# Performance work log

Hardware: AMD Instinct MI355X
Metric: run time of the kernel (lower is better)

## Reference

```python
import jax, jax.numpy as jnp
import numpy as np

B, S, D, NH, DH, L, FF, IMG, WH, DC = 4, 8320, 512, 8, 64, 4, 2048, 128, 65, 8


def _ln(x, g, b, eps=1e-5):
    m = jnp.mean(x, axis=-1, keepdims=True)
    v = jnp.mean((x - m) ** 2, axis=-1, keepdims=True)
    return (x - m) * jax.lax.rsqrt(v + eps) * g + b


def _pos_encoding(coords, d_half):
    # 2D sinusoidal PE: half channels encode col, half encode row (FIT PositionalEncoding2D)
    d_ax = d_half // 2
    div = jnp.exp(-jnp.arange(0, d_ax, 2, dtype=jnp.float32) * (np.log(10000.0) / d_ax))

    def enc(p):
        a = p[:, None].astype(jnp.float32) * div[None, :]
        return jnp.stack([jnp.sin(a), jnp.cos(a)], -1).reshape(p.shape[0], d_ax)

    return jnp.concatenate([enc(coords[:, 1]), enc(coords[:, 0])], -1)  # (S, d_half)


def setup_inputs():
    key = jax.random.key(0)
    ks = iter(jax.random.split(key, 64))
    n = lambda shape, s=0.02: jax.random.normal(next(ks), shape, jnp.float32) * s
    rows, cols = jnp.meshgrid(jnp.arange(IMG), jnp.arange(WH), indexing='ij')
    coords = jnp.stack([rows.reshape(-1), cols.reshape(-1)], -1).astype(jnp.int32)  # (S,2)
    return dict(
        x=jax.random.normal(next(ks), (B, S, 2), jnp.float32),
        fbp=jax.random.normal(next(ks), (B, S, 2), jnp.float32),
        mag_min=jnp.zeros((1,), jnp.float32),
        mag_max=jnp.ones((1,), jnp.float32),
        attenuation=jax.random.uniform(next(ks), (1, IMG, WH), jnp.float32),
        coords=coords,
        dst_flatten_coords=jnp.arange(S, dtype=jnp.int32),
        img_shape=IMG,
        emb_w=n((2, D // 2), 0.5), emb_b=jnp.zeros((D // 2,), jnp.float32),
        Wq=n((L, D, D)), bq=jnp.zeros((L, D), jnp.float32),
        Wk=n((L, D, D)), bk=jnp.zeros((L, D), jnp.float32),
        Wv=n((L, D, D)), bv=jnp.zeros((L, D), jnp.float32),
        Wo=n((L, D, D)), bo=jnp.zeros((L, D), jnp.float32),
        ln1_g=jnp.ones((L, D), jnp.float32), ln1_b=jnp.zeros((L, D), jnp.float32),
        W1=n((L, D, FF)), b1=jnp.zeros((L, FF), jnp.float32),
        W2=n((L, FF, D)), b2=jnp.zeros((L, D), jnp.float32),
        ln2_g=jnp.ones((L, D), jnp.float32), ln2_b=jnp.zeros((L, D), jnp.float32),
        lnf_g=jnp.ones((D,), jnp.float32), lnf_b=jnp.zeros((D,), jnp.float32),
        amp_w=n((D, 1)), amp_b=jnp.zeros((1,), jnp.float32),
        phase_w=n((D, 1)), phase_b=jnp.zeros((1,), jnp.float32),
        conv1_w=n((DC, 1, 3, 3), 0.1), conv1_b=jnp.zeros((DC,), jnp.float32),
        bn_g=jnp.ones((DC,), jnp.float32), bn_b=jnp.zeros((DC,), jnp.float32),
        conv2_w=n((1, DC, 1, 1), 0.1), conv2_b=jnp.zeros((1,), jnp.float32),
    )


def _conv(x, w, b, pad):
    y = jax.lax.conv_general_dilated(x, w, (1, 1), [(pad, pad), (pad, pad)],
                                     dimension_numbers=('NCHW', 'OIHW', 'NCHW'))
    return y + b[None, :, None, None]


def _forward(fbp, mag_min, mag_max, attenuation,
             emb_w, emb_b, Wq, bq, Wk, bk, Wv, bv, Wo, bo,
             ln1_g, ln1_b, W1, b1, W2, b2, ln2_g, ln2_b, lnf_g, lnf_b,
             amp_w, amp_b, phase_w, phase_b,
             conv1_w, conv1_b, bn_g, bn_b, conv2_w, conv2_b,
             coords, dst_flatten_coords, img_shape):
    pe = _pos_encoding(coords, D // 2)  # (S, D/2)
    h = jnp.concatenate([fbp @ emb_w + emb_b,
                         jnp.broadcast_to(pe, (fbp.shape[0], S, D // 2))], -1)  # (B,S,D)
    for i in range(L):
        # non-causal linear attention (fast-transformers): phi(x)=elu(x)+1
        q = (h @ Wq[i] + bq[i]).reshape(B, S, NH, DH)
        k = (h @ Wk[i] + bk[i]).reshape(B, S, NH, DH)
        v = (h @ Wv[i] + bv[i]).reshape(B, S, NH, DH)
        qf = jax.nn.elu(q) + 1.0
        kf = jax.nn.elu(k) + 1.0
        kv = jnp.einsum('bshd,bshm->bhdm', kf, v)
        z = 1.0 / (jnp.einsum('bshd,bhd->bsh', qf, kf.sum(1)) + 1e-6)
        att = jnp.einsum('bshd,bhdm,bsh->bshm', qf, kv, z).reshape(B, S, D)
        h = _ln(h + (att @ Wo[i] + bo[i]), ln1_g[i], ln1_b[i])      # post-norm
        y = jax.nn.relu(h @ W1[i] + b1[i]) @ W2[i] + b2[i]
        h = _ln(h + y, ln2_g[i], ln2_b[i])
    h = _ln(h, lnf_g, lnf_b)  # final encoder LayerNorm
    y_amp = h @ amp_w + amp_b
    y_phase = jnp.tanh(h @ phase_w + phase_b)
    y_hat = jnp.concatenate([y_amp, y_phase], -1)  # (B,S,2)
    # convert2DFT: denormalize amp/phase, scatter into flattened half-spectrum
    amp = jnp.exp((y_hat[..., 0] + 1.0) * 0.5 * (mag_max - mag_min) + mag_min)
    phi = y_hat[..., 1] * jnp.pi
    dft_flat = amp * jnp.cos(phi) + 1j * (amp * jnp.sin(phi))
    dft = jnp.zeros((B, IMG * WH), jnp.complex64).at[:, dst_flatten_coords].set(dft_flat.astype(jnp.complex64))
    dft = dft.reshape(B, IMG, WH) * attenuation
    img = jnp.fft.irfftn(dft, s=(IMG, IMG), axes=(1, 2))
    img = jnp.roll(img, (IMG // 2, IMG // 2), (1, 2))[:, None]  # (B,1,IMG,IMG)
    # conv + (training-mode) batchnorm refinement with residual
    c = jax.nn.relu(_conv(img, conv1_w, conv1_b, 1))
    m = jnp.mean(c, axis=(0, 2, 3), keepdims=True)
    var = jnp.mean((c - m) ** 2, axis=(0, 2, 3), keepdims=True)
    c = (c - m) * jax.lax.rsqrt(var + 1e-5) * bn_g[None, :, None, None] + bn_b[None, :, None, None]
    c = _conv(c, conv2_w, conv2_b, 0)
    img_post = c + img
    return y_hat, img_post[:, 0]


def reference(x, fbp, mag_min, mag_max, attenuation, coords, dst_flatten_coords, img_shape,
              emb_w, emb_b, Wq, bq, Wk, bk, Wv, bv, Wo, bo,
              ln1_g, ln1_b, W1, b1, W2, b2, ln2_g, ln2_b, lnf_g, lnf_b,
              amp_w, amp_b, phase_w, phase_b,
              conv1_w, conv1_b, bn_g, bn_b, conv2_w, conv2_b):
    # x is accepted (matches original forward signature) but unused by the module body
    return _forward(fbp, mag_min, mag_max, attenuation,
                    emb_w, emb_b, Wq, bq, Wk, bk, Wv, bv, Wo, bo,
                    ln1_g, ln1_b, W1, b1, W2, b2, ln2_g, ln2_b, lnf_g, lnf_b,
                    amp_w, amp_b, phase_w, phase_b,
                    conv1_w, conv1_b, bn_g, bn_b, conv2_w, conv2_b,
                    coords, dst_flatten_coords, img_shape)
```

## Files before the change

### kernel.cpp

```cpp
#include <hip/hip_runtime.h>
#include <math.h>

#define NB 4
#define SS 8320
#define DD 512
#define NH_ 8
#define LL 4
#define FF_ 2048
#define MTOT (NB*SS)

typedef __attribute__((ext_vector_type(8))) short short8;
typedef __attribute__((ext_vector_type(4))) float f32x4;

__device__ __forceinline__ unsigned short f2bf(float f){
  union { float f; unsigned int u; } x; x.f = f;
  unsigned int r = x.u + 0x7FFFu + ((x.u >> 16) & 1u);
  return (unsigned short)(r >> 16);
}
__device__ __forceinline__ float bf2f(unsigned short u){
  return __uint_as_float(((unsigned int)u) << 16);
}
__device__ __forceinline__ void gload_lds16(const void* g, void* l){
  __builtin_amdgcn_global_load_lds(
      (__attribute__((address_space(1))) void*)g,
      (__attribute__((address_space(3))) void*)l, 16, 0, 0);
}
__device__ __forceinline__ float wred(float v){
  #pragma unroll
  for (int o = 32; o; o >>= 1) v += __shfl_xor(v, o);
  return v;
}
__device__ __forceinline__ float block_sum256(float v){
  __shared__ float sb[4];
  #pragma unroll
  for (int o = 32; o; o >>= 1) v += __shfl_down(v, o);
  int w = threadIdx.x >> 6;
  __syncthreads();
  if ((threadIdx.x & 63) == 0) sb[w] = v;
  __syncthreads();
  return sb[0] + sb[1] + sb[2] + sb[3];
}

struct P4 { const float* p0; const float* p1; const float* p2; const float* p3; };

__global__ __launch_bounds__(256) void transpose4_kernel(P4 srcs, unsigned short* __restrict__ dst)
{
  __shared__ float tile[32][33];
  const int z = blockIdx.z;
  const float* src = (z == 0) ? srcs.p0 : (z == 1) ? srcs.p1 : (z == 2) ? srcs.p2 : srcs.p3;
  unsigned short* d = dst + (size_t)z * DD * DD;
  const int n0 = blockIdx.x * 32, k0 = blockIdx.y * 32;
  const int tx = threadIdx.x & 31, ty = threadIdx.x >> 5;
  #pragma unroll
  for (int j = 0; j < 32; j += 8) tile[ty + j][tx] = src[(size_t)(k0 + ty + j) * DD + n0 + tx];
  __syncthreads();
  #pragma unroll
  for (int j = 0; j < 32; j += 8) d[(size_t)(n0 + ty + j) * DD + k0 + tx] = f2bf(tile[tx][ty + j]);
}

__global__ __launch_bounds__(256) void transpose_bf16_kernel(
    const float* __restrict__ src, unsigned short* __restrict__ dst, int K, int N)
{
  __shared__ float tile[32][33];
  const int n0 = blockIdx.x * 32, k0 = blockIdx.y * 32;
  const int tx = threadIdx.x & 31, ty = threadIdx.x >> 5;
  #pragma unroll
  for (int j = 0; j < 32; j += 8) tile[ty + j][tx] = src[(size_t)(k0 + ty + j) * N + n0 + tx];
  __syncthreads();
  #pragma unroll
  for (int j = 0; j < 32; j += 8) dst[(size_t)(n0 + ty + j) * K + k0 + tx] = f2bf(tile[tx][ty + j]);
}

__global__ __launch_bounds__(256) void embed_kernel(
    const float* __restrict__ fbp, const int* __restrict__ coords,
    const float* __restrict__ emb_w, const float* __restrict__ emb_b,
    unsigned short* __restrict__ hb)
{
  const int row = blockIdx.x;
  const int c = threadIdx.x;
  const int s = row % SS;
  const float f0 = fbp[(size_t)row * 2], f1 = fbp[(size_t)row * 2 + 1];
  const float v0 = f0 * emb_w[c] + f1 * emb_w[256 + c] + emb_b[c];
  const int p = (c < 128) ? coords[s * 2 + 1] : coords[s * 2];
  const int c2 = c & 127;
  const int jj = c2 >> 1;
  const float dv = expf(-(float)(2 * jj) * (9.210340371976184f / 128.f));
  const float a = (float)p * dv;
  const float v1 = (c2 & 1) ? cosf(a) : sinf(a);
  const size_t base = (size_t)row * DD;
  hb[base + c] = f2bf(v0);
  hb[base + 256 + c] = f2bf(v1);
}

__global__ __launch_bounds__(256) void gemm_qkv_kernel(
    const unsigned short* __restrict__ A,
    const unsigned short* __restrict__ Bt,
    const float* __restrict__ bq_, const float* __restrict__ bk_, const float* __restrict__ bv_,
    unsigned short* __restrict__ qo, unsigned short* __restrict__ ko, unsigned short* __restrict__ vo)
{
  __shared__ __attribute__((aligned(16))) unsigned short As[128 * 64];
  __shared__ __attribute__((aligned(16))) unsigned short Bs[128 * 64];
  const int tid = threadIdx.x;
  const int lane = tid & 63, w = tid >> 6;
  const int lr = lane & 15, lg = lane >> 4;
  const int wm = w >> 1, wn = w & 1;
  const int bn = blockIdx.x, bm = blockIdx.y;
  const int which = bn >> 2;
  const unsigned short* Ag = A + (size_t)bm * 128 * DD;
  const unsigned short* Bg = Bt + (size_t)bn * 128 * DD;
  unsigned short* out = (which == 0) ? qo : (which == 1) ? ko : vo;
  const float* bias = (which == 0) ? bq_ : (which == 1) ? bk_ : bv_;
  f32x4 acc[4][4] = {};
  for (int kt = 0; kt < 8; ++kt) {
    if (kt) __syncthreads();
    const int kbase = kt << 6;
    #pragma unroll
    for (int i = 0; i < 4; ++i) {
      int cid = i * 256 + tid;
      int row = cid >> 3, c = cid & 7;
      gload_lds16(Ag + (size_t)row * DD + kbase + ((c ^ (row & 7)) << 3), (void*)(As + cid * 8));
    }
    #pragma unroll
    for (int i = 0; i < 4; ++i) {
      int cid = i * 256 + tid;
      int row = cid >> 3, c = cid & 7;
      gload_lds16(Bg + (size_t)row * DD + kbase + ((c ^ (row & 7)) << 3), (void*)(Bs + cid * 8));
    }
    __syncthreads();
    #pragma unroll
    for (int kk = 0; kk < 2; ++kk) {
      short8 af[4], bfv[4];
      #pragma unroll
      for (int f = 0; f < 4; ++f) {
        int row = wm * 64 + f * 16 + lr;
        af[f] = *(const short8*)(As + row * 64 + (((kk * 4 + lg) ^ (row & 7)) << 3));
      }
      #pragma unroll
      for (int f = 0; f < 4; ++f) {
        int row = wn * 64 + f * 16 + lr;
        bfv[f] = *(const short8*)(Bs + row * 64 + (((kk * 4 + lg) ^ (row & 7)) << 3));
      }
      #pragma unroll
      for (int fm = 0; fm < 4; ++fm)
        #pragma unroll
        for (int fn = 0; fn < 4; ++fn)
          acc[fm][fn] = __builtin_amdgcn_mfma_f32_16x16x32_bf16(af[fm], bfv[fn], acc[fm][fn], 0, 0, 0);
    }
  }
  const int elu = (which < 2);
  #pragma unroll
  for (int fm = 0; fm < 4; ++fm) {
    const int row0 = bm * 128 + wm * 64 + fm * 16 + lg * 4;
    #pragma unroll
    for (int fn = 0; fn < 4; ++fn) {
      const int col = (bn & 3) * 128 + wn * 64 + fn * 16 + lr;
      const float bv = bias[col];
      #pragma unroll
      for (int r = 0; r < 4; ++r) {
        float v = acc[fm][fn][r] + bv;
        if (elu) v = (v > 0.f) ? (v + 1.f) : expf(v);
        out[(size_t)(row0 + r) * DD + col] = f2bf(v);
      }
    }
  }
}

template<int ACT, int RES>
__global__ __launch_bounds__(256) void gemm_kernel(
    const unsigned short* __restrict__ A,
    const unsigned short* __restrict__ Bt,
    const float* __restrict__ bias,
    unsigned short* __restrict__ C,
    int N, int K, int lda, int ldb)
{
  __shared__ __attribute__((aligned(16))) unsigned short As[128 * 64];
  __shared__ __attribute__((aligned(16))) unsigned short Bs[128 * 64];
  const int tid = threadIdx.x;
  const int lane = tid & 63, w = tid >> 6;
  const int lr = lane & 15, lg = lane >> 4;
  const int wm = w >> 1, wn = w & 1;
  const int bn = blockIdx.x, bm = blockIdx.y;
  const unsigned short* Ag = A + (size_t)bm * 128 * lda;
  const unsigned short* Bg = Bt + (size_t)bn * 128 * ldb;
  f32x4 acc[4][4] = {};
  const int nkt = K >> 6;
  for (int kt = 0; kt < nkt; ++kt) {
    if (kt) __syncthreads();
    const int kbase = kt << 6;
    #pragma unroll
    for (int i = 0; i < 4; ++i) {
      int cid = i * 256 + tid;
      int row = cid >> 3, c = cid & 7;
      gload_lds16(Ag + (size_t)row * lda + kbase + ((c ^ (row & 7)) << 3), (void*)(As + cid * 8));
    }
    #pragma unroll
    for (int i = 0; i < 4; ++i) {
      int cid = i * 256 + tid;
      int row = cid >> 3, c = cid & 7;
      gload_lds16(Bg + (size_t)row * ldb + kbase + ((c ^ (row & 7)) << 3), (void*)(Bs + cid * 8));
    }
    __syncthreads();
    #pragma unroll
    for (int kk = 0; kk < 2; ++kk) {
      short8 af[4], bfv[4];
      #pragma unroll
      for (int f = 0; f < 4; ++f) {
        int row = wm * 64 + f * 16 + lr;
        af[f] = *(const short8*)(As + row * 64 + (((kk * 4 + lg) ^ (row & 7)) << 3));
      }
      #pragma unroll
      for (int f = 0; f < 4; ++f) {
        int row = wn * 64 + f * 16 + lr;
        bfv[f] = *(const short8*)(Bs + row * 64 + (((kk * 4 + lg) ^ (row & 7)) << 3));
      }
      #pragma unroll
      for (int fm = 0; fm < 4; ++fm)
        #pragma unroll
        for (int fn = 0; fn < 4; ++fn)
          acc[fm][fn] = __builtin_amdgcn_mfma_f32_16x16x32_bf16(af[fm], bfv[fn], acc[fm][fn], 0, 0, 0);
    }
  }
  #pragma unroll
  for (int fm = 0; fm < 4; ++fm) {
    const int row0 = bm * 128 + wm * 64 + fm * 16 + lg * 4;
    #pragma unroll
    for (int fn = 0; fn < 4; ++fn) {
      const int col = bn * 128 + wn * 64 + fn * 16 + lr;
      const float bv = bias[col];
      #pragma unroll
      for (int r = 0; r < 4; ++r) {
        float v = acc[fm][fn][r] + bv;
        if (ACT == 2) v = (v > 0.f) ? v : 0.f;
        const size_t idx = (size_t)(row0 + r) * N + col;
        if (RES) v += bf2f(C[idx]);
        C[idx] = f2bf(v);
      }
    }
  }
}

__global__ __launch_bounds__(256) void kv_part_kernel(
    const unsigned short* __restrict__ kb, const unsigned short* __restrict__ vb,
    float* __restrict__ kvp, float* __restrict__ ksp)
{
  __shared__ __attribute__((aligned(16))) float Kc[128][64];
  __shared__ __attribute__((aligned(16))) float Vc[128][64];
  const int ch = blockIdx.x;
  const int bh = blockIdx.y;
  const int NBH = gridDim.y;
  const int b = bh >> 3, h = bh & 7;
  const int tid = threadIdx.x;
  const int d = tid >> 2, m0 = (tid & 3) << 4;
  f32x4 a0 = {}, a1 = {}, a2 = {}, a3 = {};
  float sk = 0.f;
  for (int t = 0; t < 5; ++t) {
    if (t) __syncthreads();
    const size_t roff = ((size_t)b * SS + ch * 640 + t * 128) * DD + h * 64;
    #pragma unroll
    for (int i = 0; i < 8; ++i) {
      int e4 = i * 256 + tid;
      int r = e4 >> 4, c4 = e4 & 15;
      ushort4 kq = *(const ushort4*)(kb + roff + (size_t)r * DD + c4 * 4);
      ushort4 vq = *(const ushort4*)(vb + roff + (size_t)r * DD + c4 * 4);
      f32x4 kf4 = { bf2f(kq.x), bf2f(kq.y), bf2f(kq.z), bf2f(kq.w) };
      f32x4 vf4 = { bf2f(vq.x), bf2f(vq.y), bf2f(vq.z), bf2f(vq.w) };
      *(f32x4*)&Kc[r][c4 * 4] = kf4;
      *(f32x4*)&Vc[r][c4 * 4] = vf4;
    }
    __syncthreads();
    for (int s2 = 0; s2 < 128; ++s2) {
      const float kd = Kc[s2][d];
      const f32x4* vp = (const f32x4*)&Vc[s2][m0];
      a0 += kd * vp[0]; a1 += kd * vp[1]; a2 += kd * vp[2]; a3 += kd * vp[3];
    }
    if (tid < 64) {
      for (int s2 = 0; s2 < 128; ++s2) sk += Kc[s2][tid];
    }
  }
  float* ko = kvp + (((size_t)ch * NBH + bh) * 64 + d) * 64 + m0;
  *(f32x4*)(ko) = a0; *(f32x4*)(ko + 4) = a1; *(f32x4*)(ko + 8) = a2; *(f32x4*)(ko + 12) = a3;
  if (tid < 64) ksp[((size_t)ch * NBH + bh) * 64 + tid] = sk;
}

__global__ __launch_bounds__(256) void kv_reduce_kernel(
    const float* __restrict__ kvp, const float* __restrict__ ksp,
    unsigned short* __restrict__ kvT, float* __restrict__ ksum, int NBH)
{
  const int idx = blockIdx.x * 256 + threadIdx.x;
  const int nkv = NBH * 4096;
  if (idx < nkv) {
    const int bh = idx >> 12, dm = idx & 4095;
    const int d = dm >> 6, m = dm & 63;
    float s = 0.f;
    #pragma unroll
    for (int c = 0; c < 13; ++c) s += kvp[(((size_t)c * NBH + bh) << 12) + dm];
    kvT[(size_t)bh * 4096 + m * 64 + d] = f2bf(s);
  } else if (idx < nkv + NBH * 64) {
    const int i2 = idx - nkv;
    const int bh = i2 >> 6, d = i2 & 63;
    float s = 0.f;
    #pragma unroll
    for (int c = 0; c < 13; ++c) s += ksp[((size_t)c * NBH + bh) * 64 + d];
    ksum[i2] = s;
  }
}

__global__ __launch_bounds__(256) void z_kernel(
    const unsigned short* __restrict__ qb, const float* __restrict__ ksum,
    float* __restrict__ z, int M)
{
  const int idx = blockIdx.x * 256 + threadIdx.x;
  if (idx >= M * NH_) return;
  const int h = idx & 7;
  const int bs = idx >> 3;
  const int b = bs / SS;
  const unsigned short* q = qb + (size_t)bs * DD + h * 64;
  const float* ks = ksum + ((size_t)(b * 8 + h)) * 64;
  float acc = 0.f;
  #pragma unroll
  for (int j = 0; j < 16; ++j) {
    ushort4 qv = *(const ushort4*)(q + j * 4);
    acc += bf2f(qv.x) * ks[j * 4] + bf2f(qv.y) * ks[j * 4 + 1]
         + bf2f(qv.z) * ks[j * 4 + 2] + bf2f(qv.w) * ks[j * 4 + 3];
  }
  z[idx] = 1.f / (acc + 1e-6f);
}

__global__ __launch_bounds__(256) void attn_kernel(
    unsigned short* __restrict__ qb, const unsigned short* __restrict__ kvT,
    const float* __restrict__ z)
{
  __shared__ __attribute__((aligned(16))) unsigned short Qs[128 * 64];
  __shared__ __attribute__((aligned(16))) unsigned short Ks[64 * 64];
  const int st = blockIdx.x;
// ... 141 lines not shown
  const int tid = threadIdx.x;
  if (tid < 128) {
    float a = (float)tid * (3.14159265358979323846f / 64.f);
    ct[tid] = cosf(a); st[tid] = sinf(a);
  }
  __syncthreads();
  const int idx = blockIdx.x * 256 + tid;
  const int v = idx % 65;
  const int y = (idx / 65) & 127;
  const int b = idx / (65 * 128);
  const float* pr = dre + (size_t)b * SS + v;
  const float* pi = dimg + (size_t)b * SS + v;
  float ar = 0.f, ai = 0.f;
  for (int u = 0; u < 128; ++u) {
    int t2 = (u * y) & 127;
    float cr = ct[t2], si = st[t2];
    float xr = pr[(size_t)u * 65], xi = pi[(size_t)u * 65];
    ar += xr * cr - xi * si;
    ai += xr * si + xi * cr;
  }
  tre[idx] = ar * (1.f / 128.f);
  tim[idx] = ai * (1.f / 128.f);
}

__global__ __launch_bounds__(256) void fftB_kernel(
    const float* __restrict__ tre, const float* __restrict__ tim,
    float* __restrict__ img)
{
  __shared__ float ct[128], st[128];
  const int tid = threadIdx.x;
  if (tid < 128) {
    float a = (float)tid * (3.14159265358979323846f / 64.f);
    ct[tid] = cosf(a); st[tid] = sinf(a);
  }
  __syncthreads();
  const int idx = blockIdx.x * 256 + tid;
  const int x = idx & 127;
  const int y = (idx >> 7) & 127;
  const int b = idx >> 14;
  const float* pr = tre + ((size_t)b * 128 + y) * 65;
  const float* pi = tim + ((size_t)b * 128 + y) * 65;
  float a2 = pr[0] + ((x & 1) ? -pr[64] : pr[64]);
  for (int v = 1; v < 64; ++v) {
    int t2 = (v * x) & 127;
    a2 += 2.f * (pr[v] * ct[t2] - pi[v] * st[t2]);
  }
  a2 *= (1.f / 128.f);
  const int yy = (y + 64) & 127, xx = (x + 64) & 127;
  img[((size_t)b << 14) + (yy << 7) + xx] = a2;
}

__global__ __launch_bounds__(256) void conv1_kernel(
    const float* __restrict__ img, const float* __restrict__ w,
    const float* __restrict__ bi, float* __restrict__ c1)
{
  const int idx = blockIdx.x * 256 + threadIdx.x;
  const int x = idx & 127, y = (idx >> 7) & 127, ch = (idx >> 14) & 7, b = idx >> 17;
  const float* ip = img + ((size_t)b << 14);
  const float* wp = w + ch * 9;
  float acc = bi[ch];
  #pragma unroll
  for (int dy = -1; dy <= 1; ++dy) {
    const int yy = y + dy;
    if (yy < 0 || yy > 127) continue;
    #pragma unroll
    for (int dx = -1; dx <= 1; ++dx) {
      const int xx = x + dx;
      if (xx < 0 || xx > 127) continue;
      acc += ip[(yy << 7) + xx] * wp[(dy + 1) * 3 + (dx + 1)];
    }
  }
  c1[idx] = acc > 0.f ? acc : 0.f;
}

__global__ __launch_bounds__(256) void bn_part_kernel(
    const float* __restrict__ c1, float* __restrict__ bnp)
{
  const int ch = blockIdx.x >> 5, sl = blockIdx.x & 31;
  const int tid = threadIdx.x;
  const int n = sl * 2048 + tid * 8;
  const int b = n >> 14, i = n & 16383;
  const float* p = c1 + (((size_t)b * 8 + ch) << 14) + i;
  float4 a0 = *(const float4*)p, a1 = *(const float4*)(p + 4);
  float s = a0.x + a0.y + a0.z + a0.w + a1.x + a1.y + a1.z + a1.w;
  float sq = a0.x*a0.x + a0.y*a0.y + a0.z*a0.z + a0.w*a0.w
           + a1.x*a1.x + a1.y*a1.y + a1.z*a1.z + a1.w*a1.w;
  s = block_sum256(s);
  sq = block_sum256(sq);
  if (tid == 0) { bnp[blockIdx.x] = s; bnp[256 + blockIdx.x] = sq; }
}

__global__ __launch_bounds__(256) void bn_final_kernel(
    const float* __restrict__ bnp, float* __restrict__ stats)
{
  const int t = threadIdx.x;
  float s = bnp[t], sq = bnp[256 + t];
  #pragma unroll
  for (int o = 16; o; o >>= 1) { s += __shfl_down(s, o, 32); sq += __shfl_down(sq, o, 32); }
  if ((t & 31) == 0) {
    const int ch = t >> 5;
    const float m = s * (1.f / 65536.f);
    const float var = sq * (1.f / 65536.f) - m * m;
    stats[ch] = m;
    stats[8 + ch] = rsqrtf(var + 1e-5f);
  }
}

__global__ __launch_bounds__(256) void conv2_kernel(
    const float* __restrict__ c1, const float* __restrict__ stats,
    const float* __restrict__ bng, const float* __restrict__ bnb,
    const float* __restrict__ w2, const float* __restrict__ b2,
    const float* __restrict__ img, float* __restrict__ out)
{
  const int idx = blockIdx.x * 256 + threadIdx.x;
  const int b = idx >> 14, sp = idx & 16383;
  float acc = b2[0];
  #pragma unroll
  for (int ch = 0; ch < 8; ++ch) {
    float v = c1[(((size_t)b * 8 + ch) << 14) + sp];
    v = (v - stats[ch]) * stats[8 + ch] * bng[ch] + bnb[ch];
    acc += v * w2[ch];
  }
  out[idx] = acc + img[idx];
}

extern "C" void kernel_launch(void* const* d_in, const int* in_sizes, int n_in,
                              void* d_out, int out_size, void* d_ws, size_t ws_size,
                              hipStream_t stream)
{
  (void)in_sizes; (void)n_in; (void)out_size;
  const float* fbp = (const float*)d_in[1];
  const float* mag_min = (const float*)d_in[2];
  const float* mag_max = (const float*)d_in[3];
  const float* atten = (const float*)d_in[4];
  const int* coords = (const int*)d_in[5];
  const int* dstc = (const int*)d_in[6];
  const float* emb_w = (const float*)d_in[8];
  const float* emb_b = (const float*)d_in[9];
  const float* Wq = (const float*)d_in[10]; const float* bq = (const float*)d_in[11];
  const float* Wk = (const float*)d_in[12]; const float* bk = (const float*)d_in[13];
  const float* Wv = (const float*)d_in[14]; const float* bv = (const float*)d_in[15];
  const float* Wo = (const float*)d_in[16]; const float* bo = (const float*)d_in[17];
  const float* ln1g = (const float*)d_in[18]; const float* ln1b = (const float*)d_in[19];
  const float* W1 = (const float*)d_in[20]; const float* b1 = (const float*)d_in[21];
  const float* W2 = (const float*)d_in[22]; const float* b2 = (const float*)d_in[23];
  const float* ln2g = (const float*)d_in[24]; const float* ln2b = (const float*)d_in[25];
  const float* lnfg = (const float*)d_in[26]; const float* lnfb = (const float*)d_in[27];
  const float* aw = (const float*)d_in[28]; const float* ab = (const float*)d_in[29];
  const float* pw = (const float*)d_in[30]; const float* pb = (const float*)d_in[31];
  const float* c1w = (const float*)d_in[32]; const float* c1b = (const float*)d_in[33];
  const float* bng = (const float*)d_in[34]; const float* bnb = (const float*)d_in[35];
  const float* c2w = (const float*)d_in[36]; const float* c2b = (const float*)d_in[37];

  auto rnd = [](size_t b_) { return (b_ + 255) & ~(size_t)255; };
  const size_t SZ_M   = rnd((size_t)MTOT * DD * 2);
  const size_t SZ_Y1  = rnd((size_t)MTOT * FF_ * 2);
  const size_t SZ_WT  = rnd((size_t)4 * DD * DD * 2);
  const size_t SZ_W12 = rnd((size_t)DD * FF_ * 2);
  const size_t NEED_FULL = 4 * SZ_M + rnd((size_t)13*32*4096*4) + rnd((size_t)13*32*64*4) +
                           rnd((size_t)32*4096*2) + rnd((size_t)32*64*4) +
                           rnd((size_t)MTOT*NH_*4) + SZ_WT + 2*SZ_W12 + 4096;
  const size_t NEED_FULLY = NEED_FULL + SZ_Y1;
  const size_t NEED_FB = SZ_M + rnd((size_t)SS*DD*2) + rnd((size_t)SS*FF_*2) +
                         rnd((size_t)8*4096*2) + rnd((size_t)8*64*4) +
                         rnd((size_t)SS*NH_*4) + SZ_WT + 2*SZ_W12 + 4096;
  const int mode = (ws_size >= NEED_FULLY) ? 2 : (ws_size >= NEED_FULL) ? 1 : 0;
  if (mode == 0 && ws_size < NEED_FB) return;

  char* wsp = (char*)d_ws;
  size_t off = 0;
  auto alloc = [&](size_t bytes) -> char* { char* p = wsp + off; off += rnd(bytes); return p; };

  unsigned short *hb, *qb_, *kb_, *vb_, *y1c, *y1ded = nullptr, *kvT, *wsT, *w1T, *w2T;
  float *kvp, *ksp, *ksum, *zb;
  if (mode >= 1) {
    hb  = (unsigned short*)alloc((size_t)MTOT * DD * 2);
    qb_ = (unsigned short*)alloc((size_t)MTOT * DD * 2);
    kb_ = (unsigned short*)alloc((size_t)MTOT * DD * 2);
    vb_ = (unsigned short*)alloc((size_t)MTOT * DD * 2);
    if (mode == 2) y1ded = (unsigned short*)alloc((size_t)MTOT * FF_ * 2);
    kvp = (float*)alloc((size_t)13 * 32 * 4096 * 4);
    ksp = (float*)alloc((size_t)13 * 32 * 64 * 4);
    kvT = (unsigned short*)alloc((size_t)32 * 4096 * 2);
    ksum = (float*)alloc((size_t)32 * 64 * 4);
    zb  = (float*)alloc((size_t)MTOT * NH_ * 4);
    y1c = nullptr;
  } else {
    hb  = (unsigned short*)alloc((size_t)MTOT * DD * 2);
    qb_ = (unsigned short*)alloc((size_t)SS * DD * 2);
    unsigned short* uni = (unsigned short*)alloc((size_t)SS * FF_ * 2);
    kb_ = uni;
    vb_ = uni + (size_t)SS * DD;
    kvp = (float*)(uni + 2 * (size_t)SS * DD);
    ksp = kvp + (size_t)13 * 8 * 4096;
    kvT = (unsigned short*)alloc((size_t)8 * 4096 * 2);
    ksum = (float*)alloc((size_t)8 * 64 * 4);
    zb  = (float*)alloc((size_t)SS * NH_ * 4);
    y1c = uni;
  }
  wsT = (unsigned short*)alloc((size_t)4 * DD * DD * 2);
  w1T = (unsigned short*)alloc((size_t)DD * FF_ * 2);
  w2T = (unsigned short*)alloc((size_t)DD * FF_ * 2);

  float* dre  = (float*)qb_;
  float* dimg = dre + (size_t)NB * SS;
  float* tre  = dimg + (size_t)NB * SS;
  float* tim  = tre + (size_t)NB * 128 * 65;
  float* img  = tim + (size_t)NB * 128 * 65;
  float* c1buf = img + (size_t)NB * 128 * 128;
  float* bnp  = c1buf + (size_t)NB * 8 * 128 * 128;
  float* stats = bnp + 512;

  embed_kernel<<<MTOT, 256, 0, stream>>>(fbp, coords, emb_w, emb_b, hb);

  const int npass = (mode >= 1) ? 1 : 4;
  const int NBH = (mode >= 1) ? 32 : 8;
  const int Mrows = (mode >= 1) ? MTOT : SS;

  for (int i = 0; i < LL; ++i) {
    P4 sq4 = { Wq + (size_t)i * DD * DD, Wk + (size_t)i * DD * DD,
               Wv + (size_t)i * DD * DD, Wo + (size_t)i * DD * DD };
    transpose4_kernel<<<dim3(16, 16, 4), 256, 0, stream>>>(sq4, wsT);
    transpose_bf16_kernel<<<dim3(64, 16), 256, 0, stream>>>(W1 + (size_t)i * DD * FF_, w1T, DD, FF_);
    transpose_bf16_kernel<<<dim3(16, 64), 256, 0, stream>>>(W2 + (size_t)i * DD * FF_, w2T, FF_, DD);

    for (int p = 0; p < npass; ++p) {
      unsigned short* hbp = hb + (size_t)p * SS * DD;
      gemm_qkv_kernel<<<dim3(12, Mrows / 128), 256, 0, stream>>>(
          hbp, wsT, bq + (size_t)i * DD, bk + (size_t)i * DD, bv + (size_t)i * DD,
          qb_, kb_, vb_);
      kv_part_kernel<<<dim3(13, NBH), 256, 0, stream>>>(kb_, vb_, kvp, ksp);
      kv_reduce_kernel<<<(NBH * 4096 + NBH * 64 + 255) / 256, 256, 0, stream>>>(kvp, ksp, kvT, ksum, NBH);
      z_kernel<<<(Mrows * NH_ + 255) / 256, 256, 0, stream>>>(qb_, ksum, zb, Mrows);
      attn_kernel<<<dim3(65, NBH), 256, 0, stream>>>(qb_, kvT, zb);
      gemm_kernel<0, 1><<<dim3(4, Mrows / 128), 256, 0, stream>>>(
          qb_, wsT + (size_t)3 * DD * DD, bo + (size_t)i * DD, hbp, DD, DD, DD, DD);
      ln_wave_kernel<<<Mrows / 4, 256, 0, stream>>>(hbp, ln1g + (size_t)i * DD, ln1b + (size_t)i * DD);

      if (mode == 2) {
        gemm_kernel<2, 0><<<dim3(16, MTOT / 128), 256, 0, stream>>>(
            hb, w1T, b1 + (size_t)i * FF_, y1ded, FF_, DD, DD, DD);
        gemm_kernel<0, 1><<<dim3(4, MTOT / 128), 256, 0, stream>>>(
            y1ded, w2T, b2 + (size_t)i * DD, hb, DD, FF_, FF_, FF_);
      } else if (mode == 1) {
        unsigned short* y1half = qb_;
        for (int g2 = 0; g2 < 2; ++g2) {
          unsigned short* hbg = hb + (size_t)g2 * 2 * SS * DD;
          gemm_kernel<2, 0><<<dim3(16, 2 * SS / 128), 256, 0, stream>>>(
              hbg, w1T, b1 + (size_t)i * FF_, y1half, FF_, DD, DD, DD);
          gemm_kernel<0, 1><<<dim3(4, 2 * SS / 128), 256, 0, stream>>>(
              y1half, w2T, b2 + (size_t)i * DD, hbg, DD, FF_, FF_, FF_);
        }
      } else {
        gemm_kernel<2, 0><<<dim3(16, SS / 128), 256, 0, stream>>>(
            hbp, w1T, b1 + (size_t)i * FF_, y1c, FF_, DD, DD, DD);
        gemm_kernel<0, 1><<<dim3(4, SS / 128), 256, 0, stream>>>(
            y1c, w2T, b2 + (size_t)i * DD, hbp, DD, FF_, FF_, FF_);
      }
      ln_wave_kernel<<<Mrows / 4, 256, 0, stream>>>(hbp, ln2g + (size_t)i * DD, ln2b + (size_t)i * DD);
    }
  }

  (void)hipMemsetAsync(dre, 0, (size_t)NB * SS * 4 * 2, stream);
  head_wave_kernel<<<MTOT / 4, 256, 0, stream>>>(hb, lnfg, lnfb, aw, ab, pw, pb,
                                                 mag_min, mag_max, atten, dstc,
                                                 (float*)d_out, dre, dimg);
  fftA_kernel<<<130, 256, 0, stream>>>(dre, dimg, tre, tim);
  fftB_kernel<<<256, 256, 0, stream>>>(tre, tim, img);
  conv1_kernel<<<2048, 256, 0, stream>>>(img, c1w, c1b, c1buf);
  bn_part_kernel<<<256, 256, 0, stream>>>(c1buf, bnp);
  bn_final_kernel<<<1, 256, 0, stream>>>(bnp, stats);
  conv2_kernel<<<256, 256, 0, stream>>>(c1buf, stats, bng, bnb, c2w, c2b, img,
                                        (float*)d_out + (size_t)MTOT * 2);
}
```

Before: 2.129 ms.

## Use 256x256 tiled 512-thread GEMMs with XCD remap and hoist weight transposes

Adds new GEMM kernels with 256x256 output tiles, 512 threads, 128KB of dynamic LDS double-buffered with swizzled direct-to-LDS loads, and block-ID remapping so neighbouring tiles land on the same XCD. They replace the 128-tile QKV, output-projection and FFN GEMMs in the full-batch modes. The aim is more reuse of each loaded tile and better L2 locality. All per-layer weight transposes are hoisted into three launches before the layer loop, which adds workspace for all layers' transposed weights. Large tiles risk lower occupancy and wave-quantization tails, since MTOT/256 gives 130 row blocks.

```diff
diff --git a/kernel.cpp b/kernel.cpp
--- a/kernel.cpp
+++ b/kernel.cpp
@@ -43,11 +43,13 @@
 
 struct P4 { const float* p0; const float* p1; const float* p2; const float* p3; };
 
-__global__ __launch_bounds__(256) void transpose4_kernel(P4 srcs, unsigned short* __restrict__ dst)
+__global__ __launch_bounds__(256) void transpose_qkvo_kernel(P4 srcs, unsigned short* __restrict__ dst)
 {
   __shared__ float tile[32][33];
   const int z = blockIdx.z;
-  const float* src = (z == 0) ? srcs.p0 : (z == 1) ? srcs.p1 : (z == 2) ? srcs.p2 : srcs.p3;
+  const int layer = z >> 2, m = z & 3;
+  const float* base = (m == 0) ? srcs.p0 : (m == 1) ? srcs.p1 : (m == 2) ? srcs.p2 : srcs.p3;
+  const float* src = base + (size_t)layer * DD * DD;
   unsigned short* d = dst + (size_t)z * DD * DD;
   const int n0 = blockIdx.x * 32, k0 = blockIdx.y * 32;
   const int tx = threadIdx.x & 31, ty = threadIdx.x >> 5;
@@ -59,9 +61,11 @@
 }
 
 __global__ __launch_bounds__(256) void transpose_bf16_kernel(
-    const float* __restrict__ src, unsigned short* __restrict__ dst, int K, int N)
+    const float* __restrict__ src0, unsigned short* __restrict__ dst0, int K, int N)
 {
   __shared__ float tile[32][33];
+  const float* src = src0 + (size_t)blockIdx.z * K * N;
+  unsigned short* dst = dst0 + (size_t)blockIdx.z * K * N;
   const int n0 = blockIdx.x * 32, k0 = blockIdx.y * 32;
   const int tx = threadIdx.x & 31, ty = threadIdx.x >> 5;
   #pragma unroll
@@ -90,6 +94,188 @@
   const size_t base = (size_t)row * DD;
   hb[base + c] = f2bf(v0);
   hb[base + 256 + c] = f2bf(v1);
+}
+
+__device__ __forceinline__ void xcd_remap(int gx, int gy, int& bn, int& bm)
+{
+  const int nblk = gx * gy;
+  const int id = blockIdx.x + gx * blockIdx.y;
+  const int qd = nblk >> 3, rd = nblk & 7;
+  const int xcd = id & 7, pos = id >> 3;
+  const int nid = (xcd < rd) ? (xcd * (qd + 1) + pos)
+                             : (rd * (qd + 1) + (xcd - rd) * qd + pos);
+  bn = nid % gx; bm = nid / gx;
+}
+
+__device__ __forceinline__ void stage256(const unsigned short* __restrict__ G,
+                                         int ld, int kbase, unsigned short* L, int tid)
+{
+  #pragma unroll
+  for (int i = 0; i < 4; ++i) {
+    int s = i * 512 + tid;
+    int row = s >> 3, cs = s & 7;
+    int c = cs ^ (row & 7);
+    gload_lds16(G + (size_t)row * ld + kbase + (c << 3), (void*)(L + s * 8));
+  }
+}
+
+template<int ACT, int RES>
+__global__ __launch_bounds__(512) void gemm256_kernel(
+    const unsigned short* __restrict__ A,
+    const unsigned short* __restrict__ Bt,
+    const float* __restrict__ bias,
+    unsigned short* __restrict__ C,
+    int N, int K, int lda, int ldb)
+{
+  extern __shared__ __attribute__((aligned(16))) unsigned short smem[];
+  const int tid = threadIdx.x;
+  const int lane = tid & 63, w = tid >> 6;
+  const int lr = lane & 15, lg = lane >> 4;
+  const int wm = w >> 2, wn = w & 3;
+  int bn, bm; xcd_remap(gridDim.x, gridDim.y, bn, bm);
+  const unsigned short* Ag = A + (size_t)bm * 256 * lda;
+  const unsigned short* Bg = Bt + (size_t)bn * 256 * ldb;
+  f32x4 acc[8][4] = {};
+  const int nkt = K >> 6;
+  stage256(Ag, lda, 0, smem, tid);
+  stage256(Bg, ldb, 0, smem + 32768, tid);
+  __syncthreads();
+  for (int kt = 0; kt < nkt; ++kt) {
+    const int so = (kt & 1) << 14;
+    if (kt + 1 < nkt) {
+      const int sn = ((kt + 1) & 1) << 14;
+      stage256(Ag, lda, (kt + 1) << 6, smem + sn, tid);
+      stage256(Bg, ldb, (kt + 1) << 6, smem + 32768 + sn, tid);
+    }
+    const unsigned short* Ab = smem + so;
+    const unsigned short* Bb = smem + 32768 + so;
+    #pragma unroll
+    for (int q = 0; q < 4; ++q) {
+      const int qm = q >> 1, qn = q & 1;
+      short8 af[4][2], bf_[2][2];
+      #pragma unroll
+      for (int f = 0; f < 4; ++f) {
+        int row = wm * 128 + (qm * 4 + f) * 16 + lr;
+        #pragma unroll
+        for (int ks = 0; ks < 2; ++ks)
+          af[f][ks] = *(const short8*)(Ab + row * 64 + (((ks * 4 + lg) ^ (row & 7)) << 3));
+      }
+      #pragma unroll
+      for (int f = 0; f < 2; ++f) {
+        int row = wn * 64 + (qn * 2 + f) * 16 + lr;
+        #pragma unroll
+        for (int ks = 0; ks < 2; ++ks)
+          bf_[f][ks] = *(const short8*)(Bb + row * 64 + (((ks * 4 + lg) ^ (row & 7)) << 3));
+      }
+      __builtin_amdgcn_s_setprio(1);
+      #pragma unroll
+      for (int f = 0; f < 4; ++f)
+        #pragma unroll
+        for (int g2 = 0; g2 < 2; ++g2)
+          #pragma unroll
+          for (int ks = 0; ks < 2; ++ks)
+            acc[qm * 4 + f][qn * 2 + g2] = __builtin_amdgcn_mfma_f32_16x16x32_bf16(
+                af[f][ks], bf_[g2][ks], acc[qm * 4 + f][qn * 2 + g2], 0, 0, 0);
+      __builtin_amdgcn_s_setprio(0);
+    }
+    __syncthreads();
+  }
+  #pragma unroll
+  for (int fm = 0; fm < 8; ++fm) {
+    const int row0 = bm * 256 + wm * 128 + fm * 16 + lg * 4;
+    #pragma unroll
+    for (int fn = 0; fn < 4; ++fn) {
+      const int col = bn * 256 + wn * 64 + fn * 16 + lr;
+      const float bv = bias[col];
+      #pragma unroll
+      for (int r = 0; r < 4; ++r) {
+        float v = acc[fm][fn][r] + bv;
+        if (ACT == 2) v = (v > 0.f) ? v : 0.f;
+        const size_t idx = (size_t)(row0 + r) * N + col;
+        if (RES) v += bf2f(C[idx]);
+        C[idx] = f2bf(v);
+      }
+    }
+  }
+}
+
+__global__ __launch_bounds__(512) void qkv256_kernel(
+    const unsigned short* __restrict__ A,
+    const unsigned short* __restrict__ Bt,
+    const float* __restrict__ bq_, const float* __restrict__ bk_, const float* __restrict__ bv_,
+    unsigned short* __restrict__ qo, unsigned short* __restrict__ ko, unsigned short* __restrict__ vo)
+{
+  extern __shared__ __attribute__((aligned(16))) unsigned short smem[];
+  const int tid = threadIdx.x;
+  const int lane = tid & 63, w = tid >> 6;
+  const int lr = lane & 15, lg = lane >> 4;
+  const int wm = w >> 2, wn = w & 3;
+  int bn, bm; xcd_remap(gridDim.x, gridDim.y, bn, bm);
+  const int which = bn >> 1;
+  unsigned short* out = (which == 0) ? qo : (which == 1) ? ko : vo;
+  const float* bias = (which == 0) ? bq_ : (which == 1) ? bk_ : bv_;
+  const int elu = (which < 2);
+  const unsigned short* Ag = A + (size_t)bm * 256 * DD;
+  const unsigned short* Bg = Bt + (size_t)bn * 256 * DD;
+  f32x4 acc[8][4] = {};
+  stage256(Ag, DD, 0, smem, tid);
+  stage256(Bg, DD, 0, smem + 32768, tid);
+  __syncthreads();
+  for (int kt = 0; kt < 8; ++kt) {
+    const int so = (kt & 1) << 14;
+    if (kt + 1 < 8) {
+      const int sn = ((kt + 1) & 1) << 14;
+      stage256(Ag, DD, (kt + 1) << 6, smem + sn, tid);
+      stage256(Bg, DD, (kt + 1) << 6, smem + 32768 + sn, tid);
+    }
+    const unsigned short* Ab = smem + so;
+    const unsigned short* Bb = smem + 32768 + so;
+    #pragma unroll
+    for (int q = 0; q < 4; ++q) {
+      const int qm = q >> 1, qn = q & 1;
+      short8 af[4][2], bf_[2][2];
+      #pragma unroll
+      for (int f = 0; f < 4; ++f) {
+        int row = wm * 128 + (qm * 4 + f) * 16 + lr;
+        #pragma unroll
+        for (int ks = 0; ks < 2; ++ks)
+          af[f][ks] = *(const short8*)(Ab + row * 64 + (((ks * 4 + lg) ^ (row & 7)) << 3));
+      }
+      #pragma unroll
+      for (int f = 0; f < 2; ++f) {
+        int row = wn * 64 + (qn * 2 + f) * 16 + lr;
+        #pragma unroll
+        for (int ks = 0; ks < 2; ++ks)
+          bf_[f][ks] = *(const short8*)(Bb + row * 64 + (((ks * 4 + lg) ^ (row & 7)) << 3));
+      }
+      __builtin_amdgcn_s_setprio(1);
+      #pragma unroll
+      for (int f = 0; f < 4; ++f)
+        #pragma unroll
+        for (int g2 = 0; g2 < 2; ++g2)
+          #pragma unroll
+          for (int ks = 0; ks < 2; ++ks)
+            acc[qm * 4 + f][qn * 2 + g2] = __builtin_amdgcn_mfma_f32_16x16x32_bf16(
+                af[f][ks], bf_[g2][ks], acc[qm * 4 + f][qn * 2 + g2], 0, 0, 0);
+      __builtin_amdgcn_s_setprio(0);
+    }
+    __syncthreads();
+  }
+  #pragma unroll
+  for (int fm = 0; fm < 8; ++fm) {
+    const int row0 = bm * 256 + wm * 128 + fm * 16 + lg * 4;
+    #pragma unroll
+    for (int fn = 0; fn < 4; ++fn) {
+      const int colr = (bn & 1) * 256 + wn * 64 + fn * 16 + lr;
+      const float bv = bias[colr];
+      #pragma unroll
+      for (int r = 0; r < 4; ++r) {
+        float v = acc[fm][fn][r] + bv;
+        if (elu) v = (v > 0.f) ? (v + 1.f) : expf(v);
+        out[(size_t)(row0 + r) * DD + colr] = f2bf(v);
+      }
+    }
+  }
 }
 
 __global__ __launch_bounds__(256) void gemm_qkv_kernel(
@@ -627,18 +813,26 @@
   const float* bng = (const float*)d_in[34]; const float* bnb = (const float*)d_in[35];
   const float* c2w = (const float*)d_in[36]; const float* c2b = (const float*)d_in[37];
 
+  (void)hipFuncSetAttribute((const void*)&qkv256_kernel,
+        hipFuncAttributeMaxDynamicSharedMemorySize, 131072);
+  (void)hipFuncSetAttribute((const void*)&gemm256_kernel<0, 1>,
+        hipFuncAttributeMaxDynamicSharedMemorySize, 131072);
+  (void)hipFuncSetAttribute((const void*)&gemm256_kernel<2, 0>,
+        hipFuncAttributeMaxDynamicSharedMemorySize, 131072);
+
   auto rnd = [](size_t b_) { return (b_ + 255) & ~(size_t)255; };
-  const size_t SZ_M   = rnd((size_t)MTOT * DD * 2);
-  const size_t SZ_Y1  = rnd((size_t)MTOT * FF_ * 2);
-  const size_t SZ_WT  = rnd((size_t)4 * DD * DD * 2);
-  const size_t SZ_W12 = rnd((size_t)DD * FF_ * 2);
-  const size_t NEED_FULL = 4 * SZ_M + rnd((size_t)13*32*4096*4) + rnd((size_t)13*32*64*4) +
+  const size_t SZ_M    = rnd((size_t)MTOT * DD * 2);
+  const size_t SZ_Y1   = rnd((size_t)MTOT * FF_ * 2);
+  const size_t SZ_WQKVO= rnd((size_t)LL * 4 * DD * DD * 2);
+  const size_t SZ_W12  = rnd((size_t)LL * DD * FF_ * 2);
+  const size_t SZ_WALL = SZ_WQKVO + 2 * SZ_W12;
+  const size_t NEED_FULL = SZ_WALL + 4 * SZ_M + rnd((size_t)13*32*4096*4) + rnd((size_t)13*32*64*4) +
                            rnd((size_t)32*4096*2) + rnd((size_t)32*64*4) +
-                           rnd((size_t)MTOT*NH_*4) + SZ_WT + 2*SZ_W12 + 4096;
+                           rnd((size_t)MTOT*NH_*4) + 4096;
   const size_t NEED_FULLY = NEED_FULL + SZ_Y1;
-  const size_t NEED_FB = SZ_M + rnd((size_t)SS*DD*2) + rnd((size_t)SS*FF_*2) +
+  const size_t NEED_FB = SZ_WALL + SZ_M + rnd((size_t)SS*DD*2) + rnd((size_t)SS*FF_*2) +
                          rnd((size_t)8*4096*2) + rnd((size_t)8*64*4) +
-                         rnd((size_t)SS*NH_*4) + SZ_WT + 2*SZ_W12 + 4096;
+                         rnd((size_t)SS*NH_*4) + 4096;
   const int mode = (ws_size >= NEED_FULLY) ? 2 : (ws_size >= NEED_FULL) ? 1 : 0;
   if (mode == 0 && ws_size < NEED_FB) return;
 
@@ -646,7 +840,11 @@
   size_t off = 0;
   auto alloc = [&](size_t bytes) -> char* { char* p = wsp + off; off += rnd(bytes); return p; };
 
-  unsigned short *hb, *qb_, *kb_, *vb_, *y1c, *y1ded = nullptr, *kvT, *wsT, *w1T, *w2T;
+  unsigned short* wsTall = (unsigned short*)alloc((size_t)LL * 4 * DD * DD * 2);
+  unsigned short* w1Tall = (unsigned short*)alloc((size_t)LL * DD * FF_ * 2);
+  unsigned short* w2Tall = (unsigned short*)alloc((size_t)LL * DD * FF_ * 2);
+
+  unsigned short *hb, *qb_, *kb_, *vb_, *y1c, *y1ded = nullptr, *kvT;
   float *kvp, *ksp, *ksum, *zb;
   if (mode >= 1) {
     hb  = (unsigned short*)alloc((size_t)MTOT * DD * 2);
@@ -673,9 +871,6 @@
     zb  = (float*)alloc((size_t)SS * NH_ * 4);
     y1c = uni;
   }
-  wsT = (unsigned short*)alloc((size_t)4 * DD * DD * 2);
-  w1T = (unsigned short*)alloc((size_t)DD * FF_ * 2);
-  w2T = (unsigned short*)alloc((size_t)DD * FF_ * 2);
 
   float* dre  = (float*)qb_;
   float* dimg = dre + (size_t)NB * SS;
@@ -686,6 +881,11 @@
   float* bnp  = c1buf + (size_t)NB * 8 * 128 * 128;
   float* stats = bnp + 512;
 
+  P4 sq4 = { Wq, Wk, Wv, Wo };
+  transpose_qkvo_kernel<<<dim3(16, 16, 16), 256, 0, stream>>>(sq4, wsTall);
+  transpose_bf16_kernel<<<dim3(64, 16, 4), 256, 0, stream>>>(W1, w1Tall, DD, FF_);
+  transpose_bf16_kernel<<<dim3(16, 64, 4), 256, 0, stream>>>(W2, w2Tall, FF_, DD);
+
   embed_kernel<<<MTOT, 256, 0, stream>>>(fbp, coords, emb_w, emb_b, hb);
 
   const int npass = (mode >= 1) ? 1 : 4;
@@ -693,37 +893,46 @@
   const int Mrows = (mode >= 1) ? MTOT : SS;
 
   for (int i = 0; i < LL; ++i) {
-    P4 sq4 = { Wq + (size_t)i * DD * DD, Wk + (size_t)i * DD * DD,
-               Wv + (size_t)i * DD * DD, Wo + (size_t)i * DD * DD };
-    transpose4_kernel<<<dim3(16, 16, 4), 256, 0, stream>>>(sq4, wsT);
-    transpose_bf16_kernel<<<dim3(64, 16), 256, 0, stream>>>(W1 + (size_t)i * DD * FF_, w1T, DD, FF_);
-    transpose_bf16_kernel<<<dim3(16, 64), 256, 0, stream>>>(W2 + (size_t)i * DD * FF_, w2T, FF_, DD);
+    const unsigned short* wsT = wsTall + (size_t)i * 4 * DD * DD;
+    const unsigned short* w1T = w1Tall + (size_t)i * DD * FF_;
+    const unsigned short* w2T = w2Tall + (size_t)i * DD * FF_;
 
     for (int p = 0; p < npass; ++p) {
       unsigned short* hbp = hb + (size_t)p * SS * DD;
-      gemm_qkv_kernel<<<dim3(12, Mrows / 128), 256, 0, stream>>>(
-          hbp, wsT, bq + (size_t)i * DD, bk + (size_t)i * DD, bv + (size_t)i * DD,
-          qb_, kb_, vb_);
+      if (mode >= 1) {
+        qkv256_kernel<<<dim3(6, MTOT / 256), 512, 131072, stream>>>(
+            hbp, wsT, bq + (size_t)i * DD, bk + (size_t)i * DD, bv + (size_t)i * DD,
+            qb_, kb_, vb_);
+      } else {
+        gemm_qkv_kernel<<<dim3(12, SS / 128), 256, 0, stream>>>(
+            hbp, wsT, bq + (size_t)i * DD, bk + (size_t)i * DD, bv + (size_t)i * DD,
+            qb_, kb_, vb_);
+      }
       kv_part_kernel<<<dim3(13, NBH), 256, 0, stream>>>(kb_, vb_, kvp, ksp);
       kv_reduce_kernel<<<(NBH * 4096 + NBH * 64 + 255) / 256, 256, 0, stream>>>(kvp, ksp, kvT, ksum, NBH);
       z_kernel<<<(Mrows * NH_ + 255) / 256, 256, 0, stream>>>(qb_, ksum, zb, Mrows);
       attn_kernel<<<dim3(65, NBH), 256, 0, stream>>>(qb_, kvT, zb);
-      gemm_kernel<0, 1><<<dim3(4, Mrows / 128), 256, 0, stream>>>(
-          qb_, wsT + (size_t)3 * DD * DD, bo + (size_t)i * DD, hbp, DD, DD, DD, DD);
+      if (mode >= 1) {
+        gemm256_kernel<0, 1><<<dim3(2, MTOT / 256), 512, 131072, stream>>>(
+            qb_, wsT + (size_t)3 * DD * DD, bo + (size_t)i * DD, hbp, DD, DD, DD, DD);
+      } else {
+        gemm_kernel<0, 1><<<dim3(4, SS / 128), 256, 0, stream>>>(
+            qb_, wsT + (size_t)3 * DD * DD, bo + (size_t)i * DD, hbp, DD, DD, DD, DD);
+      }
       ln_wave_kernel<<<Mrows / 4, 256, 0, stream>>>(hbp, ln1g + (size_t)i * DD, ln1b + (size_t)i * DD);
 
       if (mode == 2) {
-        gemm_kernel<2, 0><<<dim3(16, MTOT / 128), 256, 0, stream>>>(
+        gemm256_kernel<2, 0><<<dim3(8, MTOT / 256), 512, 131072, stream>>>(
             hb, w1T, b1 + (size_t)i * FF_, y1ded, FF_, DD, DD, DD);
-        gemm_kernel<0, 1><<<dim3(4, MTOT / 128), 256, 0, stream>>>(
+        gemm256_kernel<0, 1><<<dim3(2, MTOT / 256), 512, 131072, stream>>>(
             y1ded, w2T, b2 + (size_t)i * DD, hb, DD, FF_, FF_, FF_);
       } else if (mode == 1) {
         unsigned short* y1half = qb_;
         for (int g2 = 0; g2 < 2; ++g2) {
           unsigned short* hbg = hb + (size_t)g2 * 2 * SS * DD;
-          gemm_kernel<2, 0><<<dim3(16, 2 * SS / 128), 256, 0, stream>>>(
+          gemm256_kernel<2, 0><<<dim3(8, 2 * SS / 256), 512, 131072, stream>>>(
               hbg, w1T, b1 + (size_t)i * FF_, y1half, FF_, DD, DD, DD);
-          gemm_kernel<0, 1><<<dim3(4, 2 * SS / 128), 256, 0, stream>>>(
+          gemm256_kernel<0, 1><<<dim3(2, 2 * SS / 256), 512, 131072, stream>>>(
               y1half, w2T, b2 + (size_t)i * DD, hbg, DD, FF_, FF_, FF_);
         }
       } else {
```

After: 2.373 ms. 11.4% more time.

## Hoist weight transposes out of layer loop and remap GEMM blocks across XCDs

Applied to the files above, without the earlier changes.

Transposes and converts all layers' QKVO, W1 and W2 weights to bf16 in three batched launches before the layer loop, where before there were three launches per layer. This also moves the transposed weights to the front of the workspace and raises the workspace requirement. GEMM kernels now remap block IDs so that consecutive tiles are spread across the 8 XCDs in contiguous chunks, to improve L2 locality of shared A/B tiles. Fewer launches and better cache reuse are the goals; the cost is extra workspace, which may push configurations into the fallback mode.

```diff
diff --git a/kernel.cpp b/kernel.cpp
--- a/kernel.cpp
+++ b/kernel.cpp
@@ -41,13 +41,27 @@
   return sb[0] + sb[1] + sb[2] + sb[3];
 }
 
+__device__ __forceinline__ void xcd_remap(int& bn, int& bm)
+{
+  const int gx = gridDim.x;
+  const int nblk = gx * gridDim.y;
+  const int id = blockIdx.x + gx * blockIdx.y;
+  const int qd = nblk >> 3, rd = nblk & 7;
+  const int xcd = id & 7, pos = id >> 3;
+  const int nid = (xcd < rd) ? (xcd * (qd + 1) + pos)
+                             : (rd * (qd + 1) + (xcd - rd) * qd + pos);
+  bn = nid % gx; bm = nid / gx;
+}
+
 struct P4 { const float* p0; const float* p1; const float* p2; const float* p3; };
 
-__global__ __launch_bounds__(256) void transpose4_kernel(P4 srcs, unsigned short* __restrict__ dst)
+__global__ __launch_bounds__(256) void transpose_qkvo_kernel(P4 srcs, unsigned short* __restrict__ dst)
 {
   __shared__ float tile[32][33];
   const int z = blockIdx.z;
-  const float* src = (z == 0) ? srcs.p0 : (z == 1) ? srcs.p1 : (z == 2) ? srcs.p2 : srcs.p3;
+  const int layer = z >> 2, m = z & 3;
+  const float* base = (m == 0) ? srcs.p0 : (m == 1) ? srcs.p1 : (m == 2) ? srcs.p2 : srcs.p3;
+  const float* src = base + (size_t)layer * DD * DD;
   unsigned short* d = dst + (size_t)z * DD * DD;
   const int n0 = blockIdx.x * 32, k0 = blockIdx.y * 32;
   const int tx = threadIdx.x & 31, ty = threadIdx.x >> 5;
@@ -59,9 +73,11 @@
 }
 
 __global__ __launch_bounds__(256) void transpose_bf16_kernel(
-    const float* __restrict__ src, unsigned short* __restrict__ dst, int K, int N)
+    const float* __restrict__ src0, unsigned short* __restrict__ dst0, int K, int N)
 {
   __shared__ float tile[32][33];
+  const float* src = src0 + (size_t)blockIdx.z * K * N;
+  unsigned short* dst = dst0 + (size_t)blockIdx.z * K * N;
   const int n0 = blockIdx.x * 32, k0 = blockIdx.y * 32;
   const int tx = threadIdx.x & 31, ty = threadIdx.x >> 5;
   #pragma unroll
@@ -104,7 +120,7 @@
   const int lane = tid & 63, w = tid >> 6;
   const int lr = lane & 15, lg = lane >> 4;
   const int wm = w >> 1, wn = w & 1;
-  const int bn = blockIdx.x, bm = blockIdx.y;
+  int bn, bm; xcd_remap(bn, bm);
   const int which = bn >> 2;
   const unsigned short* Ag = A + (size_t)bm * 128 * DD;
   const unsigned short* Bg = Bt + (size_t)bn * 128 * DD;
@@ -179,7 +195,7 @@
   const int lane = tid & 63, w = tid >> 6;
   const int lr = lane & 15, lg = lane >> 4;
   const int wm = w >> 1, wn = w & 1;
-  const int bn = blockIdx.x, bm = blockIdx.y;
+  int bn, bm; xcd_remap(bn, bm);
   const unsigned short* Ag = A + (size_t)bm * 128 * lda;
   const unsigned short* Bg = Bt + (size_t)bn * 128 * ldb;
   f32x4 acc[4][4] = {};
@@ -628,17 +644,18 @@
   const float* c2w = (const float*)d_in[36]; const float* c2b = (const float*)d_in[37];
 
   auto rnd = [](size_t b_) { return (b_ + 255) & ~(size_t)255; };
-  const size_t SZ_M   = rnd((size_t)MTOT * DD * 2);
-  const size_t SZ_Y1  = rnd((size_t)MTOT * FF_ * 2);
-  const size_t SZ_WT  = rnd((size_t)4 * DD * DD * 2);
-  const size_t SZ_W12 = rnd((size_t)DD * FF_ * 2);
-  const size_t NEED_FULL = 4 * SZ_M + rnd((size_t)13*32*4096*4) + rnd((size_t)13*32*64*4) +
+  const size_t SZ_M    = rnd((size_t)MTOT * DD * 2);
+  const size_t SZ_Y1   = rnd((size_t)MTOT * FF_ * 2);
+  const size_t SZ_WQKVO= rnd((size_t)LL * 4 * DD * DD * 2);
+  const size_t SZ_W12  = rnd((size_t)LL * DD * FF_ * 2);
+  const size_t SZ_WALL = SZ_WQKVO + 2 * SZ_W12;
+  const size_t NEED_FULL = SZ_WALL + 4 * SZ_M + rnd((size_t)13*32*4096*4) + rnd((size_t)13*32*64*4) +
                            rnd((size_t)32*4096*2) + rnd((size_t)32*64*4) +
-                           rnd((size_t)MTOT*NH_*4) + SZ_WT + 2*SZ_W12 + 4096;
+                           rnd((size_t)MTOT*NH_*4) + 4096;
   const size_t NEED_FULLY = NEED_FULL + SZ_Y1;
-  const size_t NEED_FB = SZ_M + rnd((size_t)SS*DD*2) + rnd((size_t)SS*FF_*2) +
+  const size_t NEED_FB = SZ_WALL + SZ_M + rnd((size_t)SS*DD*2) + rnd((size_t)SS*FF_*2) +
                          rnd((size_t)8*4096*2) + rnd((size_t)8*64*4) +
-                         rnd((size_t)SS*NH_*4) + SZ_WT + 2*SZ_W12 + 4096;
+                         rnd((size_t)SS*NH_*4) + 4096;
   const int mode = (ws_size >= NEED_FULLY) ? 2 : (ws_size >= NEED_FULL) ? 1 : 0;
   if (mode == 0 && ws_size < NEED_FB) return;
 
@@ -646,7 +663,11 @@
   size_t off = 0;
   auto alloc = [&](size_t bytes) -> char* { char* p = wsp + off; off += rnd(bytes); return p; };
 
-  unsigned short *hb, *qb_, *kb_, *vb_, *y1c, *y1ded = nullptr, *kvT, *wsT, *w1T, *w2T;
+  unsigned short* wsTall = (unsigned short*)alloc((size_t)LL * 4 * DD * DD * 2);
+  unsigned short* w1Tall = (unsigned short*)alloc((size_t)LL * DD * FF_ * 2);
+  unsigned short* w2Tall = (unsigned short*)alloc((size_t)LL * DD * FF_ * 2);
+
+  unsigned short *hb, *qb_, *kb_, *vb_, *y1c, *y1ded = nullptr, *kvT;
   float *kvp, *ksp, *ksum, *zb;
   if (mode >= 1) {
     hb  = (unsigned short*)alloc((size_t)MTOT * DD * 2);
@@ -673,9 +694,6 @@
     zb  = (float*)alloc((size_t)SS * NH_ * 4);
     y1c = uni;
   }
-  wsT = (unsigned short*)alloc((size_t)4 * DD * DD * 2);
-  w1T = (unsigned short*)alloc((size_t)DD * FF_ * 2);
-  w2T = (unsigned short*)alloc((size_t)DD * FF_ * 2);
 
   float* dre  = (float*)qb_;
   float* dimg = dre + (size_t)NB * SS;
@@ -686,6 +704,11 @@
   float* bnp  = c1buf + (size_t)NB * 8 * 128 * 128;
   float* stats = bnp + 512;
 
+  P4 sq4 = { Wq, Wk, Wv, Wo };
+  transpose_qkvo_kernel<<<dim3(16, 16, 16), 256, 0, stream>>>(sq4, wsTall);
+  transpose_bf16_kernel<<<dim3(64, 16, 4), 256, 0, stream>>>(W1, w1Tall, DD, FF_);
+  transpose_bf16_kernel<<<dim3(16, 64, 4), 256, 0, stream>>>(W2, w2Tall, FF_, DD);
+
   embed_kernel<<<MTOT, 256, 0, stream>>>(fbp, coords, emb_w, emb_b, hb);
 
   const int npass = (mode >= 1) ? 1 : 4;
@@ -693,11 +716,9 @@
   const int Mrows = (mode >= 1) ? MTOT : SS;
 
   for (int i = 0; i < LL; ++i) {
-    P4 sq4 = { Wq + (size_t)i * DD * DD, Wk + (size_t)i * DD * DD,
-               Wv + (size_t)i * DD * DD, Wo + (size_t)i * DD * DD };
-    transpose4_kernel<<<dim3(16, 16, 4), 256, 0, stream>>>(sq4, wsT);
-    transpose_bf16_kernel<<<dim3(64, 16), 256, 0, stream>>>(W1 + (size_t)i * DD * FF_, w1T, DD, FF_);
-    transpose_bf16_kernel<<<dim3(16, 64), 256, 0, stream>>>(W2 + (size_t)i * DD * FF_, w2T, FF_, DD);
+    const unsigned short* wsT = wsTall + (size_t)i * 4 * DD * DD;
+    const unsigned short* w1T = w1Tall + (size_t)i * DD * FF_;
+    const unsigned short* w2T = w2Tall + (size_t)i * DD * FF_;
 
     for (int p = 0; p < npass; ++p) {
       unsigned short* hbp = hb + (size_t)p * SS * DD;
```

After: 1.983 ms. 1.07x faster.
